# Kernel optimization log

Measured on AMD Instinct MI355X. Metric: run time of the kernel, lower is better.

The kernel has to match this reference:

```python
import jax, jax.numpy as jnp
import numpy as np

V, D, H, HA = 10000, 1024, 1024, 128  # ntoken, ninp, nhid, adapt hidden
T, B = 128, 64


def setup_inputs() -> dict:
    key = jax.random.key(0)
    ks = jax.random.split(key, 8)
    u = lambda k, sh, r: jax.random.uniform(k, sh, jnp.float32, -r, r)
    return {
        "tokens": jax.random.randint(ks[0], (T, B), 0, V, dtype=jnp.int32),
        "emb": u(ks[1], (V, D), 0.1),                 # encoder weight, uniform(-0.1,0.1)
        "Wax": u(ks[2], (D, HA), 1.0 / np.sqrt(D)),   # adapt_module input weight
        "Wah": u(ks[3], (HA, HA), 1.0 / np.sqrt(HA)), # adapt_module recurrent weight
        "bah": jnp.zeros((HA,), jnp.float32),
        "Wa": u(ks[4], (HA, 2), 1.0 / np.sqrt(HA)),   # readout -> (n, s)
        "ba": jnp.zeros((2,), jnp.float32),
        "Wih": u(ks[5], (D, H), 1.0 / np.sqrt(D)),    # gamma_rnn input weight
        "Whh": u(ks[6], (H, H), 1.0 / np.sqrt(H)),    # gamma_rnn recurrent weight
        "bh": jnp.zeros((H,), jnp.float32),
        "Wd": u(ks[7], (H, V), 0.1),                  # decoder weight, uniform(-0.1,0.1)
        "bd": jnp.zeros((V,), jnp.float32),           # decoder bias, zeros
    }


def reference(tokens, emb, Wax, Wah, bah, Wa, ba, Wih, Whh, bh, Wd, bd):
    x = emb[tokens]  # [T, B, D] embedding lookup (encoder)
    Bsz = tokens.shape[1]

    def step(carry, x_t):
        h0, h1 = carry
        # adapt_module: small RNN producing per-sample gates a = [n, s]
        h0n = jnp.tanh(x_t @ Wax + h0 @ Wah + bah)            # [B, HA]
        a = jax.nn.sigmoid(h0n @ Wa + ba)                      # [B, 2]
        n, s = a[:, 0:1], a[:, 1:2]
        # gamma_rnn: adaptive-activation vanilla RNN cell
        pre = x_t @ Wih + h1 @ Whh + bh                        # [B, H]
        h1n = (1.0 - s) * jnp.tanh(n * pre) + s * jax.nn.sigmoid(n * pre)
        return (h0n, h1n), h1n

    h0_0 = jnp.zeros((Bsz, HA), x.dtype)
    h1_0 = jnp.zeros((Bsz, H), x.dtype)
    (_, h1_final), hs = jax.lax.scan(step, (h0_0, h1_0), x)   # hs: [T, B, H]
    decoded = hs @ Wd + bd                                     # [T, B, V]
    return decoded, h1_final
```

## Files before the change

### kernel.cpp

```cpp
#include <hip/hip_runtime.h>
#include <hip/hip_bf16.h>
#include <cstdint>
#include <cstddef>

#define TSTEPS 128
#define BATCH  64
#define DDIM   1024
#define HDIM   1024
#define HADIM  128
#define VOCAB  10000
#define MROWS  (TSTEPS * BATCH)

typedef __attribute__((ext_vector_type(8))) short bf16x8;
typedef __attribute__((ext_vector_type(4))) float f32x4;

__device__ __forceinline__ unsigned short f2bf(float x) {
    unsigned int u = __float_as_uint(x);
    unsigned int r = (u + 0x7fffu + ((u >> 16) & 1u)) >> 16;
    return (unsigned short)r;
}

__global__ __launch_bounds__(256) void transpose_cast(const float* __restrict__ W,
                                                      unsigned short* __restrict__ Wt,
                                                      int R, int C) {
    __shared__ float tile[32][33];
    int tc = blockIdx.x * 32;
    int tr = blockIdx.y * 32;
    int tid = threadIdx.x;
    for (int i = 0; i < 4; i++) {
        int idx = tid + i * 256;
        int r = idx >> 5, c = idx & 31;
        float v = 0.f;
        if (tr + r < R && tc + c < C) v = W[(size_t)(tr + r) * C + tc + c];
        tile[r][c] = v;
    }
    __syncthreads();
    for (int i = 0; i < 4; i++) {
        int idx = tid + i * 256;
        int r = idx >> 5, c = idx & 31;
        if (tc + r < C && tr + c < R)
            Wt[(size_t)(tc + r) * R + tr + c] = f2bf(tile[c][r]);
    }
}

__global__ __launch_bounds__(256) void gather_cast(const int* __restrict__ tok,
                                                   const float* __restrict__ emb,
                                                   unsigned short* __restrict__ xb) {
    int i = blockIdx.x;
    int t = tok[i];
    const float4* src = (const float4*)(emb + (size_t)t * DDIM);
    float4 v = src[threadIdx.x];
    ushort4 o;
    o.x = f2bf(v.x); o.y = f2bf(v.y); o.z = f2bf(v.z); o.w = f2bf(v.w);
    ((ushort4*)(xb + (size_t)i * DDIM))[threadIdx.x] = o;
}

__global__ __launch_bounds__(256) void zero_ushort(unsigned short* p, int n) {
    int i = blockIdx.x * 256 + threadIdx.x;
    if (i < n) p[i] = 0;
}

__global__ __launch_bounds__(256) void gemm_bt_bias(const unsigned short* __restrict__ A,
                                                    const unsigned short* __restrict__ Bt,
                                                    const float* __restrict__ bias,
                                                    float* __restrict__ C,
                                                    int M, int N, int K) {
    __shared__ unsigned short As[64 * 40];
    __shared__ unsigned short Bs[64 * 40];
    int rowBase = blockIdx.y * 64;
    int colBase = blockIdx.x * 64;
    int tid = threadIdx.x;
    int wave = tid >> 6, lane = tid & 63;
    int wr = wave >> 1, wc = wave & 1;
    int quad = lane >> 4, lr = lane & 15;
    int ldRow = tid >> 2;
    int ldK = (tid & 3) * 8;
    bool bvalid = (colBase + ldRow) < N;
    const unsigned short* Ag = A + (size_t)(rowBase + ldRow) * K + ldK;
    const unsigned short* Bg = Bt + (size_t)(colBase + ldRow) * K + ldK;

    f32x4 acc[2][2] = {};
    for (int k0 = 0; k0 < K; k0 += 32) {
        uint4 av = *(const uint4*)(Ag + k0);
        uint4 bv = {};
        if (bvalid) bv = *(const uint4*)(Bg + k0);
        __syncthreads();
        *(uint4*)(As + ldRow * 40 + ldK) = av;
        *(uint4*)(Bs + ldRow * 40 + ldK) = bv;
        __syncthreads();
        bf16x8 a0 = *(const bf16x8*)(As + (wr * 32 + lr) * 40 + quad * 8);
        bf16x8 a1 = *(const bf16x8*)(As + (wr * 32 + 16 + lr) * 40 + quad * 8);
        bf16x8 b0 = *(const bf16x8*)(Bs + (wc * 32 + lr) * 40 + quad * 8);
        bf16x8 b1 = *(const bf16x8*)(Bs + (wc * 32 + 16 + lr) * 40 + quad * 8);
        acc[0][0] = __builtin_amdgcn_mfma_f32_16x16x32_bf16(a0, b0, acc[0][0], 0, 0, 0);
        acc[0][1] = __builtin_amdgcn_mfma_f32_16x16x32_bf16(a0, b1, acc[0][1], 0, 0, 0);
        acc[1][0] = __builtin_amdgcn_mfma_f32_16x16x32_bf16(a1, b0, acc[1][0], 0, 0, 0);
        acc[1][1] = __builtin_amdgcn_mfma_f32_16x16x32_bf16(a1, b1, acc[1][1], 0, 0, 0);
    }
    for (int mi = 0; mi < 2; mi++)
        for (int ni = 0; ni < 2; ni++) {
            int col = colBase + wc * 32 + ni * 16 + lr;
            if (col < N) {
                float b = bias[col];
                for (int r = 0; r < 4; r++) {
                    int row = rowBase + wr * 32 + mi * 16 + quad * 4 + r;
                    C[(size_t)row * N + col] = acc[mi][ni][r] + b;
                }
            }
        }
}

__global__ __launch_bounds__(128) void h0_chain(const float* __restrict__ Xa,
                                                const float* __restrict__ Wah,
                                                const float* __restrict__ Wa,
                                                const float* __restrict__ ba,
                                                float2* __restrict__ ns) {
    int b = blockIdx.x;
    int j = threadIdx.x;
    __shared__ float WahS[HADIM * HADIM];
    __shared__ float h0s[HADIM];
    __shared__ float red[4];
    for (int i = j; i < HADIM * HADIM; i += 128) WahS[i] = Wah[i];
    h0s[j] = 0.f;
    float wa0 = Wa[j * 2 + 0], wa1 = Wa[j * 2 + 1];
    float ba0 = ba[0], ba1 = ba[1];
    __syncthreads();
    for (int t = 0; t < TSTEPS; t++) {
        float acc = Xa[((size_t)t * BATCH + b) * HADIM + j];
        for (int k = 0; k < HADIM; k++) acc += h0s[k] * WahS[k * HADIM + j];
        float h0n = tanhf(acc);
        float p0 = h0n * wa0, p1 = h0n * wa1;
        for (int off = 32; off > 0; off >>= 1) {
            p0 += __shfl_down(p0, off);
            p1 += __shfl_down(p1, off);
        }
        int wv = j >> 6;
        if ((j & 63) == 0) { red[wv * 2 + 0] = p0; red[wv * 2 + 1] = p1; }
        __syncthreads();
        float n = 1.f / (1.f + __expf(-(red[0] + red[2] + ba0)));
        float s = 1.f / (1.f + __expf(-(red[1] + red[3] + ba1)));
        if (j == 0) ns[t * BATCH + b] = make_float2(n, s);
        h0s[j] = h0n;
        __syncthreads();
    }
}

__global__ __launch_bounds__(64) void rnn_step(const unsigned short* __restrict__ Aprev,
                                               const unsigned short* __restrict__ WhhT,
                                               const float* __restrict__ Xi_t,
                                               const float2* __restrict__ ns_t,
                                               unsigned short* __restrict__ hs_t,
                                               float* __restrict__ h1f) {
    __shared__ unsigned short As[16 * 72];
    __shared__ unsigned short Bs[16 * 72];
    int rg = blockIdx.x & 3;
    int cg = blockIdx.x >> 2;
    int lane = threadIdx.x;
    int quad = lane >> 4, lr = lane & 15;
    int ldRow = lane >> 2;
    int ldK = (lane & 3) * 16;
    const unsigned short* Ag = Aprev + (size_t)(rg * 16 + ldRow) * HDIM + ldK;
    const unsigned short* Bg = WhhT + (size_t)(cg * 16 + ldRow) * HDIM + ldK;

    f32x4 acc = {};
    uint4 a0 = *(const uint4*)(Ag);
    uint4 a1 = *(const uint4*)(Ag + 8);
    uint4 b0 = *(const uint4*)(Bg);
    uint4 b1 = *(const uint4*)(Bg + 8);
    for (int k0 = 0; k0 < HDIM; k0 += 64) {
        __syncthreads();
        *(uint4*)(As + ldRow * 72 + ldK) = a0;
        *(uint4*)(As + ldRow * 72 + ldK + 8) = a1;
        *(uint4*)(Bs + ldRow * 72 + ldK) = b0;
        *(uint4*)(Bs + ldRow * 72 + ldK + 8) = b1;
        __syncthreads();
        if (k0 + 64 < HDIM) {
            a0 = *(const uint4*)(Ag + k0 + 64);
            a1 = *(const uint4*)(Ag + k0 + 72);
            b0 = *(const uint4*)(Bg + k0 + 64);
            b1 = *(const uint4*)(Bg + k0 + 72);
        }
        bf16x8 af0 = *(const bf16x8*)(As + lr * 72 + quad * 8);
        bf16x8 bf0 = *(const bf16x8*)(Bs + lr * 72 + quad * 8);
        bf16x8 af1 = *(const bf16x8*)(As + lr * 72 + 32 + quad * 8);
        bf16x8 bf1 = *(const bf16x8*)(Bs + lr * 72 + 32 + quad * 8);
        acc = __builtin_amdgcn_mfma_f32_16x16x32_bf16(af0, bf0, acc, 0, 0, 0);
        acc = __builtin_amdgcn_mfma_f32_16x16x32_bf16(af1, bf1, acc, 0, 0, 0);
    }
    int col = cg * 16 + lr;
    for (int r = 0; r < 4; r++) {
        int brow = rg * 16 + quad * 4 + r;
        float2 g = ns_t[brow];
        float pre = acc[r] + Xi_t[(size_t)brow * HDIM + col];
        float z = g.x * pre;
        float th = tanhf(z);
        float sg = 1.f / (1.f + __expf(-z));
        float h1n = (1.f - g.y) * th + g.y * sg;
        hs_t[(size_t)brow * HDIM + col] = f2bf(h1n);
        h1f[(size_t)brow * HDIM + col] = h1n;
    }
}

extern "C" void kernel_launch(void* const* d_in, const int* in_sizes, int n_in,
                              void* d_out, int out_size, void* d_ws, size_t ws_size,
                              hipStream_t stream) {
    const int*   tokens = (const int*)d_in[0];
    const float* emb    = (const float*)d_in[1];
    const float* Wax    = (const float*)d_in[2];
    const float* Wah    = (const float*)d_in[3];
    const float* bah    = (const float*)d_in[4];
    const float* Wa     = (const float*)d_in[5];
    const float* ba     = (const float*)d_in[6];
    const float* Wih    = (const float*)d_in[7];
    const float* Whh    = (const float*)d_in[8];
    const float* bh     = (const float*)d_in[9];
    const float* Wd     = (const float*)d_in[10];
    const float* bd     = (const float*)d_in[11];
    float* out = (float*)d_out;

    char* ws = (char*)d_ws;
    size_t off = 0;
    auto alloc = [&](size_t bytes) -> void* {
        void* p = ws + off;
        off += (bytes + 255) & ~(size_t)255;
        return p;
    };
    unsigned short* WihT = (unsigned short*)alloc((size_t)HDIM * DDIM * 2);
    unsigned short* WaxT = (unsigned short*)alloc((size_t)HADIM * DDIM * 2);
    unsigned short* WhhT = (unsigned short*)alloc((size_t)HDIM * HDIM * 2);
    unsigned short* WdT  = (unsigned short*)alloc((size_t)VOCAB * HDIM * 2);
    unsigned short* xb   = (unsigned short*)alloc((size_t)MROWS * DDIM * 2);
    float*          Xi   = (float*)alloc((size_t)MROWS * HDIM * 4);
    float*          Xa   = (float*)alloc((size_t)MROWS * HADIM * 4);
    unsigned short* hs   = (unsigned short*)alloc((size_t)MROWS * HDIM * 2);
    float2*         ns   = (float2*)alloc((size_t)TSTEPS * BATCH * 8);
    unsigned short* zerosA = (unsigned short*)alloc((size_t)BATCH * HDIM * 2);
    float*          h1scr  = (float*)alloc((size_t)BATCH * HDIM * 4);

    transpose_cast<<<dim3(32, 32), 256, 0, stream>>>(Wih, WihT, DDIM, HDIM);
    transpose_cast<<<dim3(4, 32), 256, 0, stream>>>(Wax, WaxT, DDIM, HADIM);
    transpose_cast<<<dim3(32, 32), 256, 0, stream>>>(Whh, WhhT, HDIM, HDIM);
    transpose_cast<<<dim3(313, 32), 256, 0, stream>>>(Wd, WdT, HDIM, VOCAB);
    gather_cast<<<MROWS, 256, 0, stream>>>(tokens, emb, xb);
    zero_ushort<<<(BATCH * HDIM + 255) / 256, 256, 0, stream>>>(zerosA, BATCH * HDIM);
    gemm_bt_bias<<<dim3(HDIM / 64, MROWS / 64), 256, 0, stream>>>(xb, WihT, bh, Xi, MROWS, HDIM, DDIM);
    gemm_bt_bias<<<dim3(HADIM / 64, MROWS / 64), 256, 0, stream>>>(xb, WaxT, bah, Xa, MROWS, HADIM, DDIM);
    h0_chain<<<BATCH, 128, 0, stream>>>(Xa, Wah, Wa, ba, ns);
    for (int t = 0; t < TSTEPS; t++) {
        const unsigned short* Ap = (t == 0) ? zerosA : hs + (size_t)(t - 1) * BATCH * HDIM;
        float* h1f = (t == TSTEPS - 1) ? (out + (size_t)MROWS * VOCAB) : h1scr;
        rnn_step<<<256, 64, 0, stream>>>(Ap, WhhT, Xi + (size_t)t * BATCH * HDIM,
                                         ns + t * BATCH, hs + (size_t)t * BATCH * HDIM, h1f);
    }
    gemm_bt_bias<<<dim3((VOCAB + 63) / 64, MROWS / 64), 256, 0, stream>>>(hs, WdT, bd, out, MROWS, VOCAB, HDIM);
}
```

Before: 2.347 ms.

## Fuse recurrent steps into one persistent cooperative kernel with register-resident Whh

```diff
diff --git a/kernel.cpp b/kernel.cpp
--- a/kernel.cpp
+++ b/kernel.cpp
@@ -1,7 +1,10 @@
 #include <hip/hip_runtime.h>
 #include <hip/hip_bf16.h>
+#include <hip/hip_cooperative_groups.h>
 #include <cstdint>
 #include <cstddef>
+
+namespace cg = cooperative_groups;
 
 #define TSTEPS 128
 #define BATCH  64
@@ -53,11 +56,6 @@
     ushort4 o;
     o.x = f2bf(v.x); o.y = f2bf(v.y); o.z = f2bf(v.z); o.w = f2bf(v.w);
     ((ushort4*)(xb + (size_t)i * DDIM))[threadIdx.x] = o;
-}
-
-__global__ __launch_bounds__(256) void zero_ushort(unsigned short* p, int n) {
-    int i = blockIdx.x * 256 + threadIdx.x;
-    if (i < n) p[i] = 0;
 }
 
 __global__ __launch_bounds__(256) void gemm_bt_bias(const unsigned short* __restrict__ A,
@@ -145,59 +143,62 @@
     }
 }
 
-__global__ __launch_bounds__(64) void rnn_step(const unsigned short* __restrict__ Aprev,
-                                               const unsigned short* __restrict__ WhhT,
-                                               const float* __restrict__ Xi_t,
-                                               const float2* __restrict__ ns_t,
-                                               unsigned short* __restrict__ hs_t,
-                                               float* __restrict__ h1f) {
-    __shared__ unsigned short As[16 * 72];
-    __shared__ unsigned short Bs[16 * 72];
-    int rg = blockIdx.x & 3;
-    int cg = blockIdx.x >> 2;
-    int lane = threadIdx.x;
+__global__ __launch_bounds__(512, 2) void rnn_fused(
+        const unsigned short* __restrict__ WhhT,
+        const float* __restrict__ Xi,
+        const float2* __restrict__ ns,
+        unsigned short* __restrict__ hs,
+        float* __restrict__ h1f) {
+    cg::grid_group grid = cg::this_grid();
+    int cgid = blockIdx.x;
+    int wave = threadIdx.x >> 6;
+    int lane = threadIdx.x & 63;
+    int m  = wave & 3;
+    int nt = wave >> 2;
     int quad = lane >> 4, lr = lane & 15;
-    int ldRow = lane >> 2;
-    int ldK = (lane & 3) * 16;
-    const unsigned short* Ag = Aprev + (size_t)(rg * 16 + ldRow) * HDIM + ldK;
-    const unsigned short* Bg = WhhT + (size_t)(cg * 16 + ldRow) * HDIM + ldK;
-
-    f32x4 acc = {};
-    uint4 a0 = *(const uint4*)(Ag);
-    uint4 a1 = *(const uint4*)(Ag + 8);
-    uint4 b0 = *(const uint4*)(Bg);
-    uint4 b1 = *(const uint4*)(Bg + 8);
-    for (int k0 = 0; k0 < HDIM; k0 += 64) {
-        __syncthreads();
-        *(uint4*)(As + ldRow * 72 + ldK) = a0;
-        *(uint4*)(As + ldRow * 72 + ldK + 8) = a1;
-        *(uint4*)(Bs + ldRow * 72 + ldK) = b0;
-        *(uint4*)(Bs + ldRow * 72 + ldK + 8) = b1;
-        __syncthreads();
-        if (k0 + 64 < HDIM) {
-            a0 = *(const uint4*)(Ag + k0 + 64);
-            a1 = *(const uint4*)(Ag + k0 + 72);
-            b0 = *(const uint4*)(Bg + k0 + 64);
-            b1 = *(const uint4*)(Bg + k0 + 72);
-        }
-        bf16x8 af0 = *(const bf16x8*)(As + lr * 72 + quad * 8);
-        bf16x8 bf0 = *(const bf16x8*)(Bs + lr * 72 + quad * 8);
-        bf16x8 af1 = *(const bf16x8*)(As + lr * 72 + 32 + quad * 8);
-        bf16x8 bf1 = *(const bf16x8*)(Bs + lr * 72 + 32 + quad * 8);
-        acc = __builtin_amdgcn_mfma_f32_16x16x32_bf16(af0, bf0, acc, 0, 0, 0);
-        acc = __builtin_amdgcn_mfma_f32_16x16x32_bf16(af1, bf1, acc, 0, 0, 0);
-    }
-    int col = cg * 16 + lr;
-    for (int r = 0; r < 4; r++) {
-        int brow = rg * 16 + quad * 4 + r;
-        float2 g = ns_t[brow];
-        float pre = acc[r] + Xi_t[(size_t)brow * HDIM + col];
-        float z = g.x * pre;
-        float th = tanhf(z);
-        float sg = 1.f / (1.f + __expf(-z));
-        float h1n = (1.f - g.y) * th + g.y * sg;
-        hs_t[(size_t)brow * HDIM + col] = f2bf(h1n);
-        h1f[(size_t)brow * HDIM + col] = h1n;
+    int colBase = cgid * 32 + nt * 16;
+
+    bf16x8 bfr[32];
+    {
+        const unsigned short* Bg = WhhT + (size_t)(colBase + lr) * HDIM + quad * 8;
+        #pragma unroll
+        for (int kc = 0; kc < 32; kc++)
+            bfr[kc] = *(const bf16x8*)(Bg + kc * 32);
+    }
+    const int col  = colBase + lr;
+    const int arow = m * 16 + lr;
+
+    for (int t = 0; t < TSTEPS; t++) {
+        f32x4 acc = {};
+        if (t > 0) {
+            const unsigned short* Ag = hs + ((size_t)(t - 1) * BATCH + arow) * HDIM + quad * 8;
+            uint4 apf[8];
+            #pragma unroll
+            for (int i = 0; i < 8; i++) apf[i] = *(const uint4*)(Ag + i * 32);
+            #pragma unroll
+            for (int kc = 0; kc < 32; kc++) {
+                uint4 av = apf[kc & 7];
+                if (kc < 24) apf[kc & 7] = *(const uint4*)(Ag + (kc + 8) * 32);
+                acc = __builtin_amdgcn_mfma_f32_16x16x32_bf16(
+                          *(const bf16x8*)&av, bfr[kc], acc, 0, 0, 0);
+            }
+        }
+        const float*  Xt  = Xi + (size_t)t * BATCH * HDIM;
+        const float2* nst = ns + t * BATCH;
+        unsigned short* ht = hs + (size_t)t * BATCH * HDIM;
+        #pragma unroll
+        for (int r = 0; r < 4; r++) {
+            int brow = m * 16 + quad * 4 + r;
+            float2 g = nst[brow];
+            float pre = acc[r] + Xt[(size_t)brow * HDIM + col];
+            float z = g.x * pre;
+            float th = tanhf(z);
+            float sg = 1.f / (1.f + __expf(-z));
+            float h1n = (1.f - g.y) * th + g.y * sg;
+            ht[(size_t)brow * HDIM + col] = f2bf(h1n);
+            if (t == TSTEPS - 1) h1f[(size_t)brow * HDIM + col] = h1n;
+        }
+        grid.sync();
     }
 }
 
@@ -234,23 +235,23 @@
     float*          Xa   = (float*)alloc((size_t)MROWS * HADIM * 4);
     unsigned short* hs   = (unsigned short*)alloc((size_t)MROWS * HDIM * 2);
     float2*         ns   = (float2*)alloc((size_t)TSTEPS * BATCH * 8);
-    unsigned short* zerosA = (unsigned short*)alloc((size_t)BATCH * HDIM * 2);
-    float*          h1scr  = (float*)alloc((size_t)BATCH * HDIM * 4);
 
     transpose_cast<<<dim3(32, 32), 256, 0, stream>>>(Wih, WihT, DDIM, HDIM);
     transpose_cast<<<dim3(4, 32), 256, 0, stream>>>(Wax, WaxT, DDIM, HADIM);
     transpose_cast<<<dim3(32, 32), 256, 0, stream>>>(Whh, WhhT, HDIM, HDIM);
     transpose_cast<<<dim3(313, 32), 256, 0, stream>>>(Wd, WdT, HDIM, VOCAB);
     gather_cast<<<MROWS, 256, 0, stream>>>(tokens, emb, xb);
-    zero_ushort<<<(BATCH * HDIM + 255) / 256, 256, 0, stream>>>(zerosA, BATCH * HDIM);
     gemm_bt_bias<<<dim3(HDIM / 64, MROWS / 64), 256, 0, stream>>>(xb, WihT, bh, Xi, MROWS, HDIM, DDIM);
     gemm_bt_bias<<<dim3(HADIM / 64, MROWS / 64), 256, 0, stream>>>(xb, WaxT, bah, Xa, MROWS, HADIM, DDIM);
     h0_chain<<<BATCH, 128, 0, stream>>>(Xa, Wah, Wa, ba, ns);
-    for (int t = 0; t < TSTEPS; t++) {
-        const unsigned short* Ap = (t == 0) ? zerosA : hs + (size_t)(t - 1) * BATCH * HDIM;
-        float* h1f = (t == TSTEPS - 1) ? (out + (size_t)MROWS * VOCAB) : h1scr;
-        rnn_step<<<256, 64, 0, stream>>>(Ap, WhhT, Xi + (size_t)t * BATCH * HDIM,
-                                         ns + t * BATCH, hs + (size_t)t * BATCH * HDIM, h1f);
+    {
+        float* h1fin = out + (size_t)MROWS * VOCAB;
+        const unsigned short* WhhT_a = WhhT;
+        const float*  Xi_a = Xi;
+        const float2* ns_a = ns;
+        unsigned short* hs_a = hs;
+        void* args[] = { (void*)&WhhT_a, (void*)&Xi_a, (void*)&ns_a, (void*)&hs_a, (void*)&h1fin };
+        hipLaunchCooperativeKernel((const void*)rnn_fused, dim3(32), dim3(512), args, 0, stream);
     }
     gemm_bt_bias<<<dim3((VOCAB + 63) / 64, MROWS / 64), 256, 0, stream>>>(hs, WdT, bd, out, MROWS, VOCAB, HDIM);
 }
```

After: 3.179 ms. 35.5% more time.
